# Performance work log

Measured on AMD Instinct MI355X. Metric: run time of the kernel, lower is better.

The kernel has to match this reference:

```python
import jax, jax.numpy as jnp
import numpy as np

N = 100000   # nodes per type (author == paper count here)
E = 800000   # edges per edge type
D = 128      # input feature dim
HID = 128    # hidden_channels
OUT = 64     # out_channels
L = 2        # num_layers


def setup_inputs() -> dict:
    key = jax.random.key(0)
    ks = jax.random.split(key, 14)
    x_author = jax.random.normal(ks[0], (N, D), jnp.float32)
    x_paper = jax.random.normal(ks[1], (N, D), jnp.float32)
    edge_ap = jnp.stack([
        jax.random.randint(ks[2], (E,), 0, N),
        jax.random.randint(ks[3], (E,), 0, N),
    ]).astype(jnp.int32)  # [2,E] author->paper (src,dst)
    # paper->author: ensure every paper id appears as a source so the
    # meta-path conversion keeps all E edges (static shape under jit)
    pa_src = jnp.concatenate([jnp.arange(N), jax.random.randint(ks[4], (E - N,), 0, N)]).astype(jnp.int32)
    pa_dst = jax.random.randint(ks[5], (E,), 0, N).astype(jnp.int32)
    edge_pa = jnp.stack([pa_src, pa_dst])
    perm = jax.random.permutation(ks[6], N).astype(jnp.int32)  # DGI corruption
    s = 0.05
    # SAGEConv params: [layer, edge_type] with edge_type 0 = (author->paper), 1 = (paper->author)
    sage_Wl = jax.random.normal(ks[7], (L, 2, HID, D), jnp.float32) * s   # neighbor lin
    sage_Wr = jax.random.normal(ks[8], (L, 2, HID, D), jnp.float32) * s   # root lin
    sage_b = jnp.zeros((L, 2, HID), jnp.float32)
    # GATConv (heads=1) params
    gat_W = jax.random.normal(ks[9], (OUT, HID), jnp.float32) * s
    gat_att_src = jax.random.normal(ks[10], (OUT,), jnp.float32) * s
    gat_att_dst = jax.random.normal(ks[11], (OUT,), jnp.float32) * s
    gat_b = jnp.zeros((OUT,), jnp.float32)
    prelu_a = jnp.asarray(0.25, jnp.float32)
    return dict(x_author=x_author, x_paper=x_paper, sage_Wl=sage_Wl, sage_Wr=sage_Wr,
                sage_b=sage_b, gat_W=gat_W, gat_att_src=gat_att_src, gat_att_dst=gat_att_dst,
                gat_b=gat_b, prelu_a=prelu_a, edge_ap=edge_ap, edge_pa=edge_pa, perm=perm)


def _sage(x_src, x_dst, src, dst, Wl, Wr, b, n_dst):
    # SAGEConv: mean-aggregate neighbor feats, lin_l(agg) + lin_r(root) + bias
    agg = jax.ops.segment_sum(x_src[src], dst, num_segments=n_dst)       # [n_dst, D]
    cnt = jax.ops.segment_sum(jnp.ones((src.shape[0],), x_src.dtype), dst, num_segments=n_dst)
    mean = agg / jnp.maximum(cnt, 1.0)[:, None]
    return mean @ Wl.T + x_dst @ Wr.T + b


def _gat_prelu(feat, src, dst, W, a_src, a_dst, b, prelu_a, n):
    # GATConv heads=1 (self loops already appended by caller) + PReLU
    h = feat @ W.T                                                        # [n, OUT]
    e = jax.nn.leaky_relu((h @ a_src)[src] + (h @ a_dst)[dst], 0.2)       # [E']
    m = jax.ops.segment_max(e, dst, num_segments=n)
    ex = jnp.exp(e - m[dst])
    den = jax.ops.segment_sum(ex, dst, num_segments=n)
    coef = ex / den[dst]
    out = jax.ops.segment_sum(coef[:, None] * h[src], dst, num_segments=n) + b
    return jnp.where(out >= 0, out, prelu_a * out)


def reference(x_author, x_paper, sage_Wl, sage_Wr, sage_b, gat_W, gat_att_src,
              gat_att_dst, gat_b, prelu_a, edge_ap, edge_pa, perm):
    # Original loop feeds xx_dict into every layer, so only the LAST layer's
    # output survives; and only x_dict['author'] is consumed downstream.
    l = L - 1
    h_author = jax.nn.leaky_relu(
        _sage(x_paper, x_author, edge_pa[0], edge_pa[1],
              sage_Wl[l, 1], sage_Wr[l, 1], sage_b[l, 1], N), 0.01)
    # meta-path author->author edges (paper mapped via last-write paper->author dict)
    p2a = jnp.zeros((N,), jnp.int32).at[edge_pa[0]].set(edge_pa[1])
    self_loop = jnp.arange(N, dtype=jnp.int32)  # GATConv add_self_loops=True
    meta_src = jnp.concatenate([edge_ap[0], self_loop])
    meta_dst = jnp.concatenate([p2a[edge_ap[1]], self_loop])
    pos = _gat_prelu(h_author, meta_src, meta_dst, gat_W, gat_att_src, gat_att_dst, gat_b, prelu_a, N)
    neg = _gat_prelu(h_author[perm], meta_src, meta_dst, gat_W, gat_att_src, gat_att_dst, gat_b, prelu_a, N)
    summary = jnp.mean(pos, axis=0)
    return pos, neg, summary
```

## Files before the change

### kernel.cpp

```cpp
#include <hip/hip_runtime.h>
#include <stdint.h>

#define NN 100000
#define EE 800000
#define DD 128
#define HH 128
#define OO 64

#define SPA 40
#define SME 112

#define PREP_EDGE_B 3125
#define PREP_SEED_B 391
#define PREP_CAST_B 12500
#define P2_SAGE_B  25000
#define P2_CMP_B   391
#define P3_META_B  3125
#define P3_GEMM_B  782

typedef __attribute__((ext_vector_type(8))) short short8v;
typedef __attribute__((ext_vector_type(4))) float f32x4;

__device__ __forceinline__ unsigned short f2bf(float f) {
    union { float f; unsigned int u; } v; v.f = f;
    unsigned int u = v.u;
    u = (u + 0x7fffu + ((u >> 16) & 1u)) >> 16;
    return (unsigned short)u;
}
__device__ __forceinline__ float bf2f(unsigned short b) {
    union { unsigned int u; float f; } v; v.u = ((unsigned int)b) << 16;
    return v.f;
}

__global__ __launch_bounds__(256) void k_prep(const int* __restrict__ pa_src,
                                              const int* __restrict__ pa_dst,
                                              const float* __restrict__ x,
                                              int* __restrict__ amax,
                                              int* __restrict__ cnt_pa,
                                              int* __restrict__ col_pa,
                                              unsigned short* __restrict__ xbf) {
    int b = blockIdx.x, t = threadIdx.x;
    if (b < PREP_EDGE_B) {
        int e = b * 256 + t;
        if (e >= EE) return;
        int s = pa_src[e], d = pa_dst[e];
        if (e >= NN) atomicMax(&amax[s], e);
        int pos = atomicAdd(&cnt_pa[d], 1);
        if (pos < SPA) __builtin_nontemporal_store(s, &col_pa[d * SPA + pos]);
    } else if (b < PREP_EDGE_B + PREP_SEED_B) {
        int s = (b - PREP_EDGE_B) * 256 + t;
        if (s >= NN) return;
        atomicMax(&amax[s], s);
    } else {
        long i = (long)(b - PREP_EDGE_B - PREP_SEED_B) * 256 + t;
        if (i >= (long)NN * DD / 4) return;
        float4 v = ((const float4*)x)[i];
        ushort4 w;
        w.x = f2bf(v.x); w.y = f2bf(v.y); w.z = f2bf(v.z); w.w = f2bf(v.w);
        ((ushort4*)xbf)[i] = w;
    }
}

__global__ __launch_bounds__(256) void k_pack2(const int* __restrict__ cnt_pa,
                                               const int* __restrict__ col_pa,
                                               const unsigned short* __restrict__ xbf,
                                               const int* __restrict__ amax,
                                               const int* __restrict__ pa_dst,
                                               int* __restrict__ p2a32,
                                               unsigned short* __restrict__ mean_bf) {
    int b = blockIdx.x, t = threadIdx.x;
    if (b < P2_SAGE_B) {
        long gid = (long)b * 256 + t;
        int d = (int)(gid >> 6);
        if (d >= NN) return;
        int lane = (int)(gid & 63);
        int dcnt = cnt_pa[d];
        int deg = (dcnt > SPA) ? SPA : dcnt;
        const int* row = col_pa + d * SPA;
        float ax = 0.f, ay = 0.f;
        int i = 0;
        for (; i + 3 < deg; i += 4) {
            int s0 = row[i], s1 = row[i + 1], s2 = row[i + 2], s3 = row[i + 3];
            ushort2 v0 = ((const ushort2*)(xbf + (long)s0 * DD))[lane];
            ushort2 v1 = ((const ushort2*)(xbf + (long)s1 * DD))[lane];
            ushort2 v2 = ((const ushort2*)(xbf + (long)s2 * DD))[lane];
            ushort2 v3 = ((const ushort2*)(xbf + (long)s3 * DD))[lane];
            ax += (bf2f(v0.x) + bf2f(v1.x)) + (bf2f(v2.x) + bf2f(v3.x));
            ay += (bf2f(v0.y) + bf2f(v1.y)) + (bf2f(v2.y) + bf2f(v3.y));
        }
        for (; i < deg; ++i) {
            int s = row[i];
            ushort2 v = ((const ushort2*)(xbf + (long)s * DD))[lane];
            ax += bf2f(v.x);
            ay += bf2f(v.y);
        }
        float sc = 1.0f / fmaxf((float)dcnt, 1.0f);
        ushort2 w;
        w.x = f2bf(ax * sc);
        w.y = f2bf(ay * sc);
        ((ushort2*)(mean_bf + (long)d * DD))[lane] = w;
    } else {
        int s = (b - P2_SAGE_B) * 256 + t;
        if (s >= NN) return;
        p2a32[s] = pa_dst[amax[s]];
    }
}

__global__ __launch_bounds__(256) void k_sagegemm(const unsigned short* __restrict__ mean_bf,
                                                  const float* __restrict__ xa,
                                                  const float* __restrict__ Wl,
                                                  const float* __restrict__ Wr,
                                                  const float* __restrict__ sb,
                                                  unsigned short* __restrict__ h) {
    __shared__ unsigned short wlds[2][HH * DD];
    int t = threadIdx.x;
    #pragma unroll
    for (int it = 0; it < 8; ++it) {
        int cid = t + it * 256;
        int o = cid >> 4, c = cid & 15;
        int boff = (o * 256 + c * 16) ^ ((o & 7) << 4);
        {
            const float4* p = (const float4*)(Wl + (long)o * DD + c * 8);
            float4 a = p[0], b = p[1];
            short8v w;
            w[0]=(short)f2bf(a.x); w[1]=(short)f2bf(a.y); w[2]=(short)f2bf(a.z); w[3]=(short)f2bf(a.w);
            w[4]=(short)f2bf(b.x); w[5]=(short)f2bf(b.y); w[6]=(short)f2bf(b.z); w[7]=(short)f2bf(b.w);
            *(short8v*)((char*)(&wlds[0][0]) + boff) = w;
        }
        {
            const float4* p = (const float4*)(Wr + (long)o * DD + c * 8);
            float4 a = p[0], b = p[1];
            short8v w;
            w[0]=(short)f2bf(a.x); w[1]=(short)f2bf(a.y); w[2]=(short)f2bf(a.z); w[3]=(short)f2bf(a.w);
            w[4]=(short)f2bf(b.x); w[5]=(short)f2bf(b.y); w[6]=(short)f2bf(b.z); w[7]=(short)f2bf(b.w);
            *(short8v*)((char*)(&wlds[1][0]) + boff) = w;
        }
    }
    __syncthreads();

    int wave = t >> 6, lane = t & 63;
    int rowbase = blockIdx.x * 128 + wave * 32;
    int lr = lane & 15;
    int kq = (lane >> 4) * 8;
    int r0 = rowbase + lr, r1 = r0 + 16;
    int cr0 = (r0 < NN) ? r0 : 0;
    int cr1 = (r1 < NN) ? r1 : 0;

    f32x4 acc[2][8];
    #pragma unroll
    for (int i = 0; i < 2; ++i)
        #pragma unroll
        for (int j = 0; j < 8; ++j) { f32x4 z = {0.f,0.f,0.f,0.f}; acc[i][j] = z; }

    #pragma unroll
    for (int k0 = 0; k0 < DD; k0 += 32) {
        int kk = k0 + kq;
        short8v am0 = *(const short8v*)(mean_bf + (long)cr0 * DD + kk);
        short8v am1 = *(const short8v*)(mean_bf + (long)cr1 * DD + kk);
        const float4* q0 = (const float4*)(xa + (long)cr0 * DD + kk);
        const float4* q1 = (const float4*)(xa + (long)cr1 * DD + kk);
        float4 a0 = q0[0], b0 = q0[1], a1 = q1[0], b1 = q1[1];
        short8v ax0, ax1;
        ax0[0]=(short)f2bf(a0.x); ax0[1]=(short)f2bf(a0.y); ax0[2]=(short)f2bf(a0.z); ax0[3]=(short)f2bf(a0.w);
        ax0[4]=(short)f2bf(b0.x); ax0[5]=(short)f2bf(b0.y); ax0[6]=(short)f2bf(b0.z); ax0[7]=(short)f2bf(b0.w);
        ax1[0]=(short)f2bf(a1.x); ax1[1]=(short)f2bf(a1.y); ax1[2]=(short)f2bf(a1.z); ax1[3]=(short)f2bf(a1.w);
        ax1[4]=(short)f2bf(b1.x); ax1[5]=(short)f2bf(b1.y); ax1[6]=(short)f2bf(b1.z); ax1[7]=(short)f2bf(b1.w);
        #pragma unroll
        for (int nb = 0; nb < 8; ++nb) {
            int o = nb * 16 + lr;
            int boff = (o * 256 + kk * 2) ^ ((o & 7) << 4);
            short8v bl = *(const short8v*)((const char*)(&wlds[0][0]) + boff);
            short8v br = *(const short8v*)((const char*)(&wlds[1][0]) + boff);
            acc[0][nb] = __builtin_amdgcn_mfma_f32_16x16x32_bf16(am0, bl, acc[0][nb], 0, 0, 0);
            acc[1][nb] = __builtin_amdgcn_mfma_f32_16x16x32_bf16(am1, bl, acc[1][nb], 0, 0, 0);
            acc[0][nb] = __builtin_amdgcn_mfma_f32_16x16x32_bf16(ax0, br, acc[0][nb], 0, 0, 0);
            acc[1][nb] = __builtin_amdgcn_mfma_f32_16x16x32_bf16(ax1, br, acc[1][nb], 0, 0, 0);
        }
    }
    int q = lane >> 4;
    #pragma unroll
    for (int rh = 0; rh < 2; ++rh) {
        #pragma unroll
        for (int nb = 0; nb < 8; ++nb) {
            int col = nb * 16 + lr;
            float bias = sb[col];
            #pragma unroll
            for (int r = 0; r < 4; ++r) {
                int row = rowbase + rh * 16 + q * 4 + r;
                if (row < NN) {
                    float v = acc[rh][nb][r] + bias;
                    v = (v >= 0.f) ? v : 0.01f * v;
                    h[(long)row * HH + col] = f2bf(v);
                }
            }
        }
    }
}

__global__ __launch_bounds__(256) void k_pack3(const int* __restrict__ ap_src,
                                               const int* __restrict__ ap_dst,
                                               const int* __restrict__ p2a32,
                                               int* __restrict__ cnt_meta,
                                               int* __restrict__ col_meta,
                                               const unsigned short* __restrict__ h,
                                               const float* __restrict__ Wg,
                                               const float* __restrict__ asrc,
                                               const float* __restrict__ adst,
                                               unsigned short* __restrict__ hg,
                                               float* __restrict__ al_s,
                                               float* __restrict__ al_d) {
    __shared__ unsigned short wlds[OO * HH];
    int b = blockIdx.x, t = threadIdx.x;
    if (b < P3_META_B) {
        int e = b * 256 + t;
        if (e >= EE) return;
        int d = p2a32[ap_dst[e]];
        int pos = atomicAdd(&cnt_meta[d], 1);
        if (pos < SME) __builtin_nontemporal_store(ap_src[e], &col_meta[d * SME + pos]);
        return;
    }
    int bb = b - P3_META_B;
    #pragma unroll
    for (int it = 0; it < 4; ++it) {
        int cid = t + it * 256;
        int o = cid >> 4, c = cid & 15;
        int boff = (o * 256 + c * 16) ^ ((o & 7) << 4);
        const float4* p = (const float4*)(Wg + (long)o * HH + c * 8);
        float4 a = p[0], bv = p[1];
        short8v w;
        w[0]=(short)f2bf(a.x); w[1]=(short)f2bf(a.y); w[2]=(short)f2bf(a.z); w[3]=(short)f2bf(a.w);
        w[4]=(short)f2bf(bv.x); w[5]=(short)f2bf(bv.y); w[6]=(short)f2bf(bv.z); w[7]=(short)f2bf(bv.w);
        *(short8v*)((char*)(&wlds[0]) + boff) = w;
    }
    __syncthreads();

    int wave = t >> 6, lane = t & 63;
    int rowbase = bb * 128 + wave * 32;
    int lr = lane & 15;
    int kq = (lane >> 4) * 8;
    int r0 = rowbase + lr, r1 = r0 + 16;
    int cr0 = (r0 < NN) ? r0 : 0;
    int cr1 = (r1 < NN) ? r1 : 0;

    f32x4 acc[2][4];
    #pragma unroll
    for (int i = 0; i < 2; ++i)
        #pragma unroll
        for (int j = 0; j < 4; ++j) { f32x4 z = {0.f,0.f,0.f,0.f}; acc[i][j] = z; }

    #pragma unroll
    for (int k0 = 0; k0 < HH; k0 += 32) {
        int kk = k0 + kq;
        short8v a0 = *(const short8v*)(h + (long)cr0 * HH + kk);
        short8v a1 = *(const short8v*)(h + (long)cr1 * HH + kk);
        #pragma unroll
        for (int nb = 0; nb < 4; ++nb) {
            int o = nb * 16 + lr;
            int boff = (o * 256 + kk * 2) ^ ((o & 7) << 4);
            short8v bv = *(const short8v*)((const char*)(&wlds[0]) + boff);
            acc[0][nb] = __builtin_amdgcn_mfma_f32_16x16x32_bf16(a0, bv, acc[0][nb], 0, 0, 0);
            acc[1][nb] = __builtin_amdgcn_mfma_f32_16x16x32_bf16(a1, bv, acc[1][nb], 0, 0, 0);
        }
    }
    int q = lane >> 4;
    float a_s[4], a_d[4];
    #pragma unroll
    for (int nb = 0; nb < 4; ++nb) { a_s[nb] = asrc[nb * 16 + lr]; a_d[nb] = adst[nb * 16 + lr]; }
    #pragma unroll
    for (int rh = 0; rh < 2; ++rh) {
        float ss[4] = {0.f,0.f,0.f,0.f}, dd[4] = {0.f,0.f,0.f,0.f};
        #pragma unroll
        for (int nb = 0; nb < 4; ++nb) {
            #pragma unroll
            for (int r = 0; r < 4; ++r) {
                int row = rowbase + rh * 16 + q * 4 + r;
                unsigned short wb = f2bf(acc[rh][nb][r]);
                if (row < NN) hg[(long)row * OO + nb * 16 + lr] = wb;
                float w = bf2f(wb);
                ss[r] += w * a_s[nb];
                dd[r] += w * a_d[nb];
            }
        }
        #pragma unroll
        for (int r = 0; r < 4; ++r) {
            float s = ss[r], dv = dd[r];
            #pragma unroll
            for (int off = 1; off < 16; off <<= 1) {
                s  += __shfl_xor(s,  off, 64);
                dv += __shfl_xor(dv, off, 64);
            }
            int row = rowbase + rh * 16 + q * 4 + r;
            if (lr == 0 && row < NN) { al_s[row] = s; al_d[row] = dv; }
        }
    }
}

__global__ __launch_bounds__(256) void k_gat_gather(const int* __restrict__ cnt_meta,
                                                    const int* __restrict__ col_meta,
                                                    const int* __restrict__ perm,
                                                    const float* __restrict__ al_s,
                                                    const float* __restrict__ al_d,
                                                    const unsigned short* __restrict__ hg,
                                                    const float* __restrict__ gb,
                                                    const float* __restrict__ prelu_a,
                                                    float* __restrict__ out) {
    long gid = (long)blockIdx.x * 256 + threadIdx.x;
    int d = (int)(gid >> 6);
    if (d >= NN) return;
    int j = (int)(gid & 63);
    int deg = cnt_meta[d];
    if (deg > SME) deg = SME;
    const int* row = col_meta + d * SME;
    int pd = perm[d];
    float add = al_d[d];
    float adn = al_d[pd];
    float lp = al_s[d] + add;   lp = (lp >= 0.f) ? lp : 0.2f * lp;
    float ln = al_s[pd] + adn;  ln = (ln >= 0.f) ? ln : 0.2f * ln;
    float xps = __expf(lp), xns = __expf(ln);
    float denp = xps, denn = xns;
    float accp = xps * bf2f(hg[((long)d << 6) + j]);
    float accn = xns * bf2f(hg[((long)pd << 6) + j]);

    for (int base = 0; base < deg; base += 64) {
        int cnt = deg - base;
        if (cnt > 64) cnt = 64;
        int s = 0, ps = 0;
        float xp = 0.f, xn = 0.f;
        if (j < cnt) {
            s = row[base + j];
            ps = perm[s];
            float l0 = al_s[s] + add;   l0 = (l0 >= 0.f) ? l0 : 0.2f * l0;
            xp = __expf(l0);
            float m0 = al_s[ps] + adn;  m0 = (m0 >= 0.f) ? m0 : 0.2f * m0;
            xn = __expf(m0);
        }
        float tp = xp, tn = xn;
        #pragma unroll
        for (int off = 32; off; off >>= 1) {
            tp += __shfl_xor(tp, off, 64);
            tn += __shfl_xor(tn, off, 64);
        }
        denp += tp;
        denn += tn;
        int e = 0;
        for (; e + 3 < cnt; e += 4) {
            int s0 = __shfl(s, e),   s1 = __shfl(s, e + 1),   s2 = __shfl(s, e + 2),   s3 = __shfl(s, e + 3);
            int p0 = __shfl(ps, e),  p1 = __shfl(ps, e + 1),  p2 = __shfl(ps, e + 2),  p3 = __shfl(ps, e + 3);
            float a0 = __shfl(xp, e), a1 = __shfl(xp, e + 1), a2 = __shfl(xp, e + 2), a3 = __shfl(xp, e + 3);
            float b0 = __shfl(xn, e), b1 = __shfl(xn, e + 1), b2 = __shfl(xn, e + 2), b3 = __shfl(xn, e + 3);
            float h0 = bf2f(hg[((long)s0 << 6) + j]);
            float h1 = bf2f(hg[((long)s1 << 6) + j]);
            float h2 = bf2f(hg[((long)s2 << 6) + j]);
            float h3 = bf2f(hg[((long)s3 << 6) + j]);
            float g0 = bf2f(hg[((long)p0 << 6) + j]);
            float g1 = bf2f(hg[((long)p1 << 6) + j]);
            float g2 = bf2f(hg[((long)p2 << 6) + j]);
            float g3 = bf2f(hg[((long)p3 << 6) + j]);
            accp += (a0 * h0 + a1 * h1) + (a2 * h2 + a3 * h3);
            accn += (b0 * g0 + b1 * g1) + (b2 * g2 + b3 * g3);
        }
        for (; e < cnt; ++e) {
            int sb = __shfl(s, e);
            int pb = __shfl(ps, e);
            float ab = __shfl(xp, e);
            float bb = __shfl(xn, e);
            accp += ab * bf2f(hg[((long)sb << 6) + j]);
            accn += bb * bf2f(hg[((long)pb << 6) + j]);
        }
    }
    float bias = gb[j];
    float a = prelu_a[0];
    float vp = accp / denp + bias;
    vp = (vp >= 0.f) ? vp : a * vp;
    out[((long)d << 6) + j] = vp;
    float vn = accn / denn + bias;
    vn = (vn >= 0.f) ? vn : a * vn;
    out[((long)(NN + d) << 6) + j] = vn;
}

__global__ __launch_bounds__(256) void k_summary(const float* __restrict__ out_pos,
                                                 float* __restrict__ summary) {
    int t = threadIdx.x;
    int j = t & 63, sub = t >> 6;
    float acc = 0.f;
    for (int row = blockIdx.x * 4 + sub; row < NN; row += 256 * 4) {
        acc += out_pos[(long)row * OO + j];
    }
    __shared__ float red[4][OO];
    red[sub][j] = acc;
    __syncthreads();
    if (sub == 0) {
        float ttl = red[0][j] + red[1][j] + red[2][j] + red[3][j];
        atomicAdd(summary + j, ttl * (1.0f / NN));
    }
}

extern "C" void kernel_launch(void* const* d_in, const int* in_sizes, int n_in,
                              void* d_out, int out_size, void* d_ws, size_t ws_size,
                              hipStream_t stream) {
    const float* x_author = (const float*)d_in[0];
    const float* x_paper  = (const float*)d_in[1];
    const float* sage_Wl  = (const float*)d_in[2];
    const float* sage_Wr  = (const float*)d_in[3];
    const float* sage_b   = (const float*)d_in[4];
    const float* gat_W    = (const float*)d_in[5];
    const float* gat_as   = (const float*)d_in[6];
    const float* gat_ad   = (const float*)d_in[7];
    const float* gat_b    = (const float*)d_in[8];
    const float* prelu_a  = (const float*)d_in[9];
    const int*   edge_ap  = (const int*)d_in[10];
    const int*   edge_pa  = (const int*)d_in[11];
    const int*   perm     = (const int*)d_in[12];

    char* ws = (char*)d_ws;
    int*   cnt_pa    = (int*)(ws + 0);
    int*   cnt_meta  = (int*)(ws + 400000);
    int*   amax      = (int*)(ws + 800000);
    int*   p2a32     = (int*)(ws + 1200000);
    float* al_s      = (float*)(ws + 1600000);
    float* al_d      = (float*)(ws + 2000000);
    int*   col_pa    = (int*)(ws + 2400000);
    unsigned short* xbf     = (unsigned short*)(ws + 18400000);
    unsigned short* mean_bf = (unsigned short*)(ws + 44000000);
    int*   col_meta  = (int*)(ws + 44000000);
    unsigned short* h  = xbf;
    unsigned short* hg = (unsigned short*)col_pa;

    hipMemsetAsync(d_ws, 0, 1200000, stream);
    hipMemsetAsync((char*)d_out + (size_t)2 * NN * OO * sizeof(float), 0,
                   OO * sizeof(float), stream);

    const float* Wl = sage_Wl + 3 * HH * DD;
    const float* Wr = sage_Wr + 3 * HH * DD;
    const float* sb = sage_b  + 3 * HH;

    k_prep<<<PREP_EDGE_B + PREP_SEED_B + PREP_CAST_B, 256, 0, stream>>>(
        edge_pa, edge_pa + EE, x_paper, amax, cnt_pa, col_pa, xbf);
    k_pack2<<<P2_SAGE_B + P2_CMP_B, 256, 0, stream>>>(
        cnt_pa, col_pa, xbf, amax, edge_pa + EE, p2a32, mean_bf);
    k_sagegemm<<<P3_GEMM_B, 256, 0, stream>>>(mean_bf, x_author, Wl, Wr, sb, h);
    k_pack3<<<P3_META_B + P3_GEMM_B, 256, 0, stream>>>(
        edge_ap, edge_ap + EE, p2a32, cnt_meta, col_meta,
        h, gat_W, gat_as, gat_ad, hg, al_s, al_d);
    k_gat_gather<<<(NN * 64 + 255) / 256, 256, 0, stream>>>(cnt_meta, col_meta, perm,
                                                            al_s, al_d, hg, gat_b, prelu_a,
                                                            (float*)d_out);
    k_summary<<<256, 256, 0, stream>>>((float*)d_out, (float*)d_out + 2L * NN * OO);
}
```

Baseline: 359.8 us.

## Fuse SAGE and GAT GEMMs via LDS, precast weights to bf16 in prep

The SAGE GEMM and the GAT projection GEMM now run in one kernel. The intermediate h tile stays in swizzled LDS instead of going through global memory. Weight casting to bf16 moves into the prep kernel, and the GEMM reads B fragments straight from global/L2 instead of staging them in LDS. The separate seed atomicMax pass is folded into the edge pass. This saves a kernel launch and the h round-trip, but risks slower B-operand reads from global memory and shifts the workspace layout.

```diff
diff --git a/kernel.cpp b/kernel.cpp
--- a/kernel.cpp
+++ b/kernel.cpp
@@ -10,13 +10,13 @@
 #define SPA 40
 #define SME 112
 
-#define PREP_EDGE_B 3125
-#define PREP_SEED_B 391
-#define PREP_CAST_B 12500
-#define P2_SAGE_B  25000
-#define P2_CMP_B   391
-#define P3_META_B  3125
-#define P3_GEMM_B  782
+#define PREP_EDGE_B  3125
+#define PREP_CASTX_B 12500
+#define PREP_CASTW_B 40
+#define P2_SAGE_B    25000
+#define P2_CMP_B     391
+#define P3_GEMM_B    782
+#define P3_META_B    3125
 
 typedef __attribute__((ext_vector_type(8))) short short8v;
 typedef __attribute__((ext_vector_type(4))) float f32x4;
@@ -35,29 +35,39 @@
 __global__ __launch_bounds__(256) void k_prep(const int* __restrict__ pa_src,
                                               const int* __restrict__ pa_dst,
                                               const float* __restrict__ x,
+                                              const float* __restrict__ Wl,
+                                              const float* __restrict__ Wr,
+                                              const float* __restrict__ Wg,
                                               int* __restrict__ amax,
                                               int* __restrict__ cnt_pa,
                                               int* __restrict__ col_pa,
-                                              unsigned short* __restrict__ xbf) {
+                                              unsigned short* __restrict__ xbf,
+                                              unsigned short* __restrict__ wbf) {
     int b = blockIdx.x, t = threadIdx.x;
     if (b < PREP_EDGE_B) {
         int e = b * 256 + t;
         if (e >= EE) return;
         int s = pa_src[e], d = pa_dst[e];
-        if (e >= NN) atomicMax(&amax[s], e);
+        atomicMax(&amax[s], e);
         int pos = atomicAdd(&cnt_pa[d], 1);
         if (pos < SPA) __builtin_nontemporal_store(s, &col_pa[d * SPA + pos]);
-    } else if (b < PREP_EDGE_B + PREP_SEED_B) {
-        int s = (b - PREP_EDGE_B) * 256 + t;
-        if (s >= NN) return;
-        atomicMax(&amax[s], s);
-    } else {
-        long i = (long)(b - PREP_EDGE_B - PREP_SEED_B) * 256 + t;
+    } else if (b < PREP_EDGE_B + PREP_CASTX_B) {
+        long i = (long)(b - PREP_EDGE_B) * 256 + t;
         if (i >= (long)NN * DD / 4) return;
         float4 v = ((const float4*)x)[i];
         ushort4 w;
         w.x = f2bf(v.x); w.y = f2bf(v.y); w.z = f2bf(v.z); w.w = f2bf(v.w);
         ((ushort4*)xbf)[i] = w;
+    } else {
+        int i4 = (b - PREP_EDGE_B - PREP_CASTX_B) * 256 + t;
+        if (i4 >= 10240) return;
+        float4 v;
+        if (i4 < 4096)       v = ((const float4*)Wl)[i4];
+        else if (i4 < 8192)  v = ((const float4*)Wr)[i4 - 4096];
+        else                 v = ((const float4*)Wg)[i4 - 8192];
+        ushort4 w;
+        w.x = f2bf(v.x); w.y = f2bf(v.y); w.z = f2bf(v.z); w.w = f2bf(v.w);
+        ((ushort4*)wbf)[i4] = w;
     }
 }
 
@@ -106,42 +116,38 @@
     }
 }
 
-__global__ __launch_bounds__(256) void k_sagegemm(const unsigned short* __restrict__ mean_bf,
-                                                  const float* __restrict__ xa,
-                                                  const float* __restrict__ Wl,
-                                                  const float* __restrict__ Wr,
-                                                  const float* __restrict__ sb,
-                                                  unsigned short* __restrict__ h) {
-    __shared__ unsigned short wlds[2][HH * DD];
-    int t = threadIdx.x;
-    #pragma unroll
-    for (int it = 0; it < 8; ++it) {
-        int cid = t + it * 256;
-        int o = cid >> 4, c = cid & 15;
-        int boff = (o * 256 + c * 16) ^ ((o & 7) << 4);
-        {
-            const float4* p = (const float4*)(Wl + (long)o * DD + c * 8);
-            float4 a = p[0], b = p[1];
-            short8v w;
-            w[0]=(short)f2bf(a.x); w[1]=(short)f2bf(a.y); w[2]=(short)f2bf(a.z); w[3]=(short)f2bf(a.w);
-            w[4]=(short)f2bf(b.x); w[5]=(short)f2bf(b.y); w[6]=(short)f2bf(b.z); w[7]=(short)f2bf(b.w);
-            *(short8v*)((char*)(&wlds[0][0]) + boff) = w;
-        }
-        {
-            const float4* p = (const float4*)(Wr + (long)o * DD + c * 8);
-            float4 a = p[0], b = p[1];
-            short8v w;
-            w[0]=(short)f2bf(a.x); w[1]=(short)f2bf(a.y); w[2]=(short)f2bf(a.z); w[3]=(short)f2bf(a.w);
-            w[4]=(short)f2bf(b.x); w[5]=(short)f2bf(b.y); w[6]=(short)f2bf(b.z); w[7]=(short)f2bf(b.w);
-            *(short8v*)((char*)(&wlds[1][0]) + boff) = w;
-        }
-    }
-    __syncthreads();
-
+__global__ __launch_bounds__(256) void k_pack3(const unsigned short* __restrict__ mean_bf,
+                                               const float* __restrict__ xa,
+                                               const unsigned short* __restrict__ wbf,
+                                               const float* __restrict__ sb,
+                                               const float* __restrict__ asrc,
+                                               const float* __restrict__ adst,
+                                               unsigned short* __restrict__ hg,
+                                               float* __restrict__ al_s,
+                                               float* __restrict__ al_d,
+                                               const int* __restrict__ ap_src,
+                                               const int* __restrict__ ap_dst,
+                                               const int* __restrict__ p2a32,
+                                               int* __restrict__ cnt_meta,
+                                               int* __restrict__ col_meta) {
+    __shared__ unsigned short hs[4 * 32 * 128];
+    int b = blockIdx.x, t = threadIdx.x;
+    if (b >= P3_GEMM_B) {
+        int e = (b - P3_GEMM_B) * 256 + t;
+        if (e >= EE) return;
+        int d = p2a32[ap_dst[e]];
+        int pos = atomicAdd(&cnt_meta[d], 1);
+        if (pos < SME) __builtin_nontemporal_store(ap_src[e], &col_meta[d * SME + pos]);
+        return;
+    }
+    const unsigned short* wl = wbf;
+    const unsigned short* wr = wbf + 16384;
+    const unsigned short* wg = wbf + 32768;
     int wave = t >> 6, lane = t & 63;
-    int rowbase = blockIdx.x * 128 + wave * 32;
+    int rowbase = b * 128 + wave * 32;
     int lr = lane & 15;
-    int kq = (lane >> 4) * 8;
+    int q = lane >> 4;
+    int kq = q * 8;
     int r0 = rowbase + lr, r1 = r0 + 16;
     int cr0 = (r0 < NN) ? r0 : 0;
     int cr1 = (r1 < NN) ? r1 : 0;
@@ -168,16 +174,15 @@
         #pragma unroll
         for (int nb = 0; nb < 8; ++nb) {
             int o = nb * 16 + lr;
-            int boff = (o * 256 + kk * 2) ^ ((o & 7) << 4);
-            short8v bl = *(const short8v*)((const char*)(&wlds[0][0]) + boff);
-            short8v br = *(const short8v*)((const char*)(&wlds[1][0]) + boff);
+            short8v bl = *(const short8v*)(wl + o * DD + kk);
+            short8v br = *(const short8v*)(wr + o * DD + kk);
             acc[0][nb] = __builtin_amdgcn_mfma_f32_16x16x32_bf16(am0, bl, acc[0][nb], 0, 0, 0);
             acc[1][nb] = __builtin_amdgcn_mfma_f32_16x16x32_bf16(am1, bl, acc[1][nb], 0, 0, 0);
             acc[0][nb] = __builtin_amdgcn_mfma_f32_16x16x32_bf16(ax0, br, acc[0][nb], 0, 0, 0);
             acc[1][nb] = __builtin_amdgcn_mfma_f32_16x16x32_bf16(ax1, br, acc[1][nb], 0, 0, 0);
         }
     }
-    int q = lane >> 4;
+    char* hbase = (char*)hs + wave * 8192;
     #pragma unroll
     for (int rh = 0; rh < 2; ++rh) {
         #pragma unroll
@@ -186,83 +191,34 @@
             float bias = sb[col];
             #pragma unroll
             for (int r = 0; r < 4; ++r) {
-                int row = rowbase + rh * 16 + q * 4 + r;
-                if (row < NN) {
-                    float v = acc[rh][nb][r] + bias;
-                    v = (v >= 0.f) ? v : 0.01f * v;
-                    h[(long)row * HH + col] = f2bf(v);
-                }
+                int lrow = rh * 16 + q * 4 + r;
+                float v = acc[rh][nb][r] + bias;
+                v = (v >= 0.f) ? v : 0.01f * v;
+                int boff = (lrow * 256 + col * 2) ^ ((lrow & 7) << 4);
+                *(unsigned short*)(hbase + boff) = f2bf(v);
             }
         }
     }
-}
-
-__global__ __launch_bounds__(256) void k_pack3(const int* __restrict__ ap_src,
-                                               const int* __restrict__ ap_dst,
-                                               const int* __restrict__ p2a32,
-                                               int* __restrict__ cnt_meta,
-                                               int* __restrict__ col_meta,
-                                               const unsigned short* __restrict__ h,
-                                               const float* __restrict__ Wg,
-                                               const float* __restrict__ asrc,
-                                               const float* __restrict__ adst,
-                                               unsigned short* __restrict__ hg,
-                                               float* __restrict__ al_s,
-                                               float* __restrict__ al_d) {
-    __shared__ unsigned short wlds[OO * HH];
-    int b = blockIdx.x, t = threadIdx.x;
-    if (b < P3_META_B) {
-        int e = b * 256 + t;
-        if (e >= EE) return;
-        int d = p2a32[ap_dst[e]];
-        int pos = atomicAdd(&cnt_meta[d], 1);
-        if (pos < SME) __builtin_nontemporal_store(ap_src[e], &col_meta[d * SME + pos]);
-        return;
-    }
-    int bb = b - P3_META_B;
-    #pragma unroll
-    for (int it = 0; it < 4; ++it) {
-        int cid = t + it * 256;
-        int o = cid >> 4, c = cid & 15;
-        int boff = (o * 256 + c * 16) ^ ((o & 7) << 4);
-        const float4* p = (const float4*)(Wg + (long)o * HH + c * 8);
-        float4 a = p[0], bv = p[1];
-        short8v w;
-        w[0]=(short)f2bf(a.x); w[1]=(short)f2bf(a.y); w[2]=(short)f2bf(a.z); w[3]=(short)f2bf(a.w);
-        w[4]=(short)f2bf(bv.x); w[5]=(short)f2bf(bv.y); w[6]=(short)f2bf(bv.z); w[7]=(short)f2bf(bv.w);
-        *(short8v*)((char*)(&wlds[0]) + boff) = w;
-    }
-    __syncthreads();
-
-    int wave = t >> 6, lane = t & 63;
-    int rowbase = bb * 128 + wave * 32;
-    int lr = lane & 15;
-    int kq = (lane >> 4) * 8;
-    int r0 = rowbase + lr, r1 = r0 + 16;
-    int cr0 = (r0 < NN) ? r0 : 0;
-    int cr1 = (r1 < NN) ? r1 : 0;
-
-    f32x4 acc[2][4];
+    f32x4 acc2[2][4];
     #pragma unroll
     for (int i = 0; i < 2; ++i)
         #pragma unroll
-        for (int j = 0; j < 4; ++j) { f32x4 z = {0.f,0.f,0.f,0.f}; acc[i][j] = z; }
+        for (int j = 0; j < 4; ++j) { f32x4 z = {0.f,0.f,0.f,0.f}; acc2[i][j] = z; }
 
     #pragma unroll
     for (int k0 = 0; k0 < HH; k0 += 32) {
         int kk = k0 + kq;
-        short8v a0 = *(const short8v*)(h + (long)cr0 * HH + kk);
-        short8v a1 = *(const short8v*)(h + (long)cr1 * HH + kk);
+        int boff0 = (lr * 256 + kk * 2) ^ ((lr & 7) << 4);
+        int boff1 = ((16 + lr) * 256 + kk * 2) ^ ((lr & 7) << 4);
+        short8v a0 = *(const short8v*)(hbase + boff0);
+        short8v a1 = *(const short8v*)(hbase + boff1);
         #pragma unroll
         for (int nb = 0; nb < 4; ++nb) {
-            int o = nb * 16 + lr;
-            int boff = (o * 256 + kk * 2) ^ ((o & 7) << 4);
-            short8v bv = *(const short8v*)((const char*)(&wlds[0]) + boff);
-            acc[0][nb] = __builtin_amdgcn_mfma_f32_16x16x32_bf16(a0, bv, acc[0][nb], 0, 0, 0);
-            acc[1][nb] = __builtin_amdgcn_mfma_f32_16x16x32_bf16(a1, bv, acc[1][nb], 0, 0, 0);
-        }
-    }
-    int q = lane >> 4;
+            short8v bg = *(const short8v*)(wg + (nb * 16 + lr) * HH + kk);
+            acc2[0][nb] = __builtin_amdgcn_mfma_f32_16x16x32_bf16(a0, bg, acc2[0][nb], 0, 0, 0);
+            acc2[1][nb] = __builtin_amdgcn_mfma_f32_16x16x32_bf16(a1, bg, acc2[1][nb], 0, 0, 0);
+        }
+    }
     float a_s[4], a_d[4];
     #pragma unroll
     for (int nb = 0; nb < 4; ++nb) { a_s[nb] = asrc[nb * 16 + lr]; a_d[nb] = adst[nb * 16 + lr]; }
@@ -274,7 +230,7 @@
             #pragma unroll
             for (int r = 0; r < 4; ++r) {
                 int row = rowbase + rh * 16 + q * 4 + r;
-                unsigned short wb = f2bf(acc[rh][nb][r]);
+                unsigned short wb = f2bf(acc2[rh][nb][r]);
                 if (row < NN) hg[(long)row * OO + nb * 16 + lr] = wb;
                 float w = bf2f(wb);
                 ss[r] += w * a_s[nb];
@@ -360,11 +316,11 @@
             accn += (b0 * g0 + b1 * g1) + (b2 * g2 + b3 * g3);
         }
         for (; e < cnt; ++e) {
-            int sb = __shfl(s, e);
+            int sb2 = __shfl(s, e);
             int pb = __shfl(ps, e);
             float ab = __shfl(xp, e);
             float bb = __shfl(xn, e);
-            accp += ab * bf2f(hg[((long)sb << 6) + j]);
+            accp += ab * bf2f(hg[((long)sb2 << 6) + j]);
             accn += bb * bf2f(hg[((long)pb << 6) + j]);
         }
     }
@@ -419,11 +375,11 @@
     int*   p2a32     = (int*)(ws + 1200000);
     float* al_s      = (float*)(ws + 1600000);
     float* al_d      = (float*)(ws + 2000000);
-    int*   col_pa    = (int*)(ws + 2400000);
-    unsigned short* xbf     = (unsigned short*)(ws + 18400000);
-    unsigned short* mean_bf = (unsigned short*)(ws + 44000000);
-    int*   col_meta  = (int*)(ws + 44000000);
-    unsigned short* h  = xbf;
+    unsigned short* wbf = (unsigned short*)(ws + 2400000);
+    int*   col_pa    = (int*)(ws + 2481920);
+    unsigned short* mean_bf = (unsigned short*)(ws + 18481920);
+    unsigned short* xbf     = (unsigned short*)(ws + 44081920);
+    int*   col_meta  = (int*)(ws + 44081920);
     unsigned short* hg = (unsigned short*)col_pa;
 
     hipMemsetAsync(d_ws, 0, 1200000, stream);
@@ -434,14 +390,13 @@
     const float* Wr = sage_Wr + 3 * HH * DD;
     const float* sb = sage_b  + 3 * HH;
 
-    k_prep<<<PREP_EDGE_B + PREP_SEED_B + PREP_CAST_B, 256, 0, stream>>>(
-        edge_pa, edge_pa + EE, x_paper, amax, cnt_pa, col_pa, xbf);
+    k_prep<<<PREP_EDGE_B + PREP_CASTX_B + PREP_CASTW_B, 256, 0, stream>>>(
+        edge_pa, edge_pa + EE, x_paper, Wl, Wr, gat_W, amax, cnt_pa, col_pa, xbf, wbf);
     k_pack2<<<P2_SAGE_B + P2_CMP_B, 256, 0, stream>>>(
         cnt_pa, col_pa, xbf, amax, edge_pa + EE, p2a32, mean_bf);
-    k_sagegemm<<<P3_GEMM_B, 256, 0, stream>>>(mean_bf, x_author, Wl, Wr, sb, h);
-    k_pack3<<<P3_META_B + P3_GEMM_B, 256, 0, stream>>>(
-        edge_ap, edge_ap + EE, p2a32, cnt_meta, col_meta,
-        h, gat_W, gat_as, gat_ad, hg, al_s, al_d);
+    k_pack3<<<P3_GEMM_B + P3_META_B, 256, 0, stream>>>(
+        mean_bf, x_author, wbf, sb, gat_as, gat_ad, hg, al_s, al_d,
+        edge_ap, edge_ap + EE, p2a32, cnt_meta, col_meta);
     k_gat_gather<<<(NN * 64 + 255) / 256, 256, 0, stream>>>(cnt_meta, col_meta, perm,
                                                             al_s, al_d, hg, gat_b, prelu_a,
                                                             (float*)d_out);
```

Measured after the change: 339.4 us. 1.06x faster.
